# Performance work log

Hardware: AMD Instinct MI355X
Metric: run time of the kernel (lower is better)

## Reference

```python
import jax, jax.numpy as jnp
import numpy as np

IN_C = 64
OUT_C = 64
K = 3
STRIDE = 1
PAD = 1
GROUP = 1
P = 8.0
EPS = 1e-30  # guard for all-zero patch-minus-weight (never hit with randn data)


def unfold(x, k, pad, stride):
    # Torch F.unfold: output [B, C*k*k, L] with feature ordering (c, kh, kw).
    B, C, H, W = x.shape
    xp = jnp.pad(x, ((0, 0), (0, 0), (pad, pad), (pad, pad)))
    Ho = (H + 2 * pad - k) // stride + 1
    Wo = (W + 2 * pad - k) // stride + 1
    patches = jnp.stack(
        [xp[:, :, i:i + stride * Ho:stride, j:j + stride * Wo:stride]
         for i in range(k) for j in range(k)],
        axis=2,
    )  # [B, C, k*k, Ho, Wo]
    return patches.reshape(B, C * k * k, Ho * Wo), Ho, Wo


def setup_inputs() -> dict:
    key = jax.random.key(0)
    kx, kw = jax.random.split(key)
    x = jax.random.normal(kx, (2, IN_C, 32, 32), dtype=jnp.float32)
    # weight init: randn, then identity_init sets center tap to -10
    weight = jax.random.normal(kw, (OUT_C, IN_C // GROUP, K, K), dtype=jnp.float32)
    idx = jnp.arange(OUT_C)
    weight = weight.at[idx, idx % (IN_C // GROUP), K // 2, K // 2].set(-10.0)
    bias = jnp.zeros((OUT_C,), dtype=jnp.float32)
    return {"x": x, "weight": weight, "bias": bias}


def reference(x, weight, bias):
    B = x.shape[0]
    xu, Ho, Wo = unfold(x, K, PAD, STRIDE)          # [B, Cin*k*k, L]
    Kdim = (IN_C // GROUP) * K * K
    L = xu.shape[-1]
    xg = xu.reshape(B, GROUP, 1, Kdim, L)           # [B, g, 1, Kdim, L]
    wg = weight.reshape(GROUP, OUT_C // GROUP, Kdim, 1)  # [g, O/g, Kdim, 1]
    diff = jnp.abs(xg - wg)                          # [B, g, O/g, Kdim, L]
    # stable Lp norm via L-inf normalization (normalize is detached, as in torch)
    norm_inf = jax.lax.stop_gradient(jnp.max(diff, axis=3, keepdims=True))
    scaled = diff / jnp.maximum(norm_inf, EPS)
    y = jnp.sum(scaled ** P, axis=3, keepdims=True) ** (1.0 / P) * norm_inf
    y = y.reshape(B, OUT_C, Ho, Wo)
    return y + bias[None, :, None, None]
```

## Files before the change

kernel.cpp:

```cpp
#include <hip/hip_runtime.h>

#define IN_C 64
#define OUT_C 64
#define HW 32
#define PH 34

__global__ void pad_kernel(const float* __restrict__ x, float* __restrict__ xp) {
    int i = blockIdx.x * blockDim.x + threadIdx.x;
    const int total = 2 * IN_C * PH * PH;
    if (i >= total) return;
    int col = i % PH;
    int row = (i / PH) % PH;
    int bc  = i / (PH * PH);
    float v = 0.0f;
    if (row >= 1 && row <= HW && col >= 1 && col <= HW)
        v = x[bc * HW * HW + (row - 1) * HW + (col - 1)];
    xp[i] = v;
}

__global__ void wtr_kernel(const float* __restrict__ w, float* __restrict__ wt) {
    int i = blockIdx.x * blockDim.x + threadIdx.x;
    const int total = 576 * 64;
    if (i >= total) return;
    int o = i & 63;
    int ckk = i >> 6;
    wt[i] = w[o * 576 + ckk];
}

__global__ __launch_bounds__(256, 2) void norm_conv_kernel(
    const float* __restrict__ xp, const float* __restrict__ wt,
    const float* __restrict__ bias, float* __restrict__ out) {
    int bid = blockIdx.x;
    int tile = bid & 15;
    int og = (bid >> 4) & 15;
    int b = bid >> 8;

    int tid = threadIdx.x;
    int sp = tid & 63;
    int cs = __builtin_amdgcn_readfirstlane(tid >> 6);
    int row = sp >> 5, col = sp & 31;
    int oh = tile * 2 + row;
    int ow = col;

    const float* xb = xp + ((size_t)(b * IN_C + cs * 16) * PH + oh) * PH + ow;
    const float* wb = wt + (size_t)(cs * 16) * 9 * 64 + og * 4;

    float s0 = 0.f, s1 = 0.f, s2 = 0.f, s3 = 0.f;

    for (int c = 0; c < 16; ++c) {
        const float* xr = xb + c * (PH * PH);
        const float* wr = wb + c * (9 * 64);
#pragma unroll
        for (int kh = 0; kh < 3; ++kh) {
#pragma unroll
            for (int kw = 0; kw < 3; ++kw) {
                float xv = xr[kh * PH + kw];
                float4 wv = *(const float4*)(wr + (kh * 3 + kw) * 64);
                float d0 = xv - wv.x;
                float d1 = xv - wv.y;
                float d2 = xv - wv.z;
                float d3 = xv - wv.w;
                d0 *= d0; d0 *= d0; s0 = fmaf(d0, d0, s0);
                d1 *= d1; d1 *= d1; s1 = fmaf(d1, d1, s1);
                d2 *= d2; d2 *= d2; s2 = fmaf(d2, d2, s2);
                d3 *= d3; d3 *= d3; s3 = fmaf(d3, d3, s3);
            }
        }
    }

    __shared__ float lds[4 * 64 * 4];
    ((float4*)lds)[tid] = make_float4(s0, s1, s2, s3);
    __syncthreads();

    int oi = tid >> 6;
    int sp2 = tid & 63;
    float sum = lds[(0 * 64 + sp2) * 4 + oi] + lds[(1 * 64 + sp2) * 4 + oi] +
                lds[(2 * 64 + sp2) * 4 + oi] + lds[(3 * 64 + sp2) * 4 + oi];

    float y = exp2f(0.125f * log2f(sum));
    int o = og * 4 + oi;
    int oh2 = tile * 2 + (sp2 >> 5);
    int ow2 = sp2 & 31;
    out[((b * OUT_C + o) * HW + oh2) * HW + ow2] = y + bias[o];
}

extern "C" void kernel_launch(void* const* d_in, const int* in_sizes, int n_in,
                              void* d_out, int out_size, void* d_ws, size_t ws_size,
                              hipStream_t stream) {
    const float* x = (const float*)d_in[0];
    const float* w = (const float*)d_in[1];
    const float* bias = (const float*)d_in[2];
    float* out = (float*)d_out;

    float* xp = (float*)d_ws;
    float* wt = xp + 2 * IN_C * PH * PH;

    {
        int total = 2 * IN_C * PH * PH;
        pad_kernel<<<(total + 255) / 256, 256, 0, stream>>>(x, xp);
    }
    {
        int total = 576 * 64;
        wtr_kernel<<<(total + 255) / 256, 256, 0, stream>>>(w, wt);
    }
    norm_conv_kernel<<<512, 256, 0, stream>>>(xp, wt, bias, out);
}
```

Baseline: 70.12 us.

## Fuse padding and weight transpose into conv kernel with LDS staging

Removes the separate pad and weight-transpose kernels and performs both inside a single kernel. Each block stages a padded 4-row input halo for all 64 channels and its 4 output channels' weights in shared memory. Blocks grow to 512 threads with 8 channel slices, and the partial sums are reduced through padded LDS. This cuts two kernel launches and the global workspace round-trip. In exchange, every block redundantly loads its input halo, and LDS use per block is larger, which may limit occupancy.

```diff
diff --git a/kernel.cpp b/kernel.cpp
--- a/kernel.cpp
+++ b/kernel.cpp
@@ -3,59 +3,61 @@
 #define IN_C 64
 #define OUT_C 64
 #define HW 32
-#define PH 34
 
-__global__ void pad_kernel(const float* __restrict__ x, float* __restrict__ xp) {
-    int i = blockIdx.x * blockDim.x + threadIdx.x;
-    const int total = 2 * IN_C * PH * PH;
-    if (i >= total) return;
-    int col = i % PH;
-    int row = (i / PH) % PH;
-    int bc  = i / (PH * PH);
-    float v = 0.0f;
-    if (row >= 1 && row <= HW && col >= 1 && col <= HW)
-        v = x[bc * HW * HW + (row - 1) * HW + (col - 1)];
-    xp[i] = v;
-}
+#define XS_ELEMS (64 * 4 * 36)
+#define WS_ELEMS (576 * 4)
+#define RED_ELEMS (8 * 64 * 5)
 
-__global__ void wtr_kernel(const float* __restrict__ w, float* __restrict__ wt) {
-    int i = blockIdx.x * blockDim.x + threadIdx.x;
-    const int total = 576 * 64;
-    if (i >= total) return;
-    int o = i & 63;
-    int ckk = i >> 6;
-    wt[i] = w[o * 576 + ckk];
-}
+__global__ __launch_bounds__(512, 4) void norm_conv_fused(
+    const float* __restrict__ x, const float* __restrict__ w,
+    const float* __restrict__ bias, float* __restrict__ out) {
+    __shared__ float smem[XS_ELEMS + WS_ELEMS + RED_ELEMS];
+    float* xs = smem;
+    float* wsm = smem + XS_ELEMS;
+    float* red = wsm + WS_ELEMS;
 
-__global__ __launch_bounds__(256, 2) void norm_conv_kernel(
-    const float* __restrict__ xp, const float* __restrict__ wt,
-    const float* __restrict__ bias, float* __restrict__ out) {
     int bid = blockIdx.x;
     int tile = bid & 15;
     int og = (bid >> 4) & 15;
     int b = bid >> 8;
+    int tid = threadIdx.x;
 
-    int tid = threadIdx.x;
+    for (int i = tid; i < 576 * 4; i += 512) {
+        int och = i / 576;
+        int ckk = i - och * 576;
+        wsm[ckk * 4 + och] = w[(og * 4 + och) * 576 + ckk];
+    }
+
+    for (int i = tid; i < 64 * 4 * 34; i += 512) {
+        int c = i / 136;
+        int rem = i - c * 136;
+        int r = rem / 34;
+        int pc = rem - r * 34;
+        int gr = tile * 2 - 1 + r;
+        int gc = pc - 1;
+        float v = 0.0f;
+        if (gr >= 0 && gr < HW && gc >= 0 && gc < HW)
+            v = x[((b * IN_C + c) * HW + gr) * HW + gc];
+        xs[(c * 4 + r) * 36 + pc] = v;
+    }
+    __syncthreads();
+
     int sp = tid & 63;
-    int cs = __builtin_amdgcn_readfirstlane(tid >> 6);
+    int cs = tid >> 6;
     int row = sp >> 5, col = sp & 31;
-    int oh = tile * 2 + row;
-    int ow = col;
-
-    const float* xb = xp + ((size_t)(b * IN_C + cs * 16) * PH + oh) * PH + ow;
-    const float* wb = wt + (size_t)(cs * 16) * 9 * 64 + og * 4;
 
     float s0 = 0.f, s1 = 0.f, s2 = 0.f, s3 = 0.f;
 
-    for (int c = 0; c < 16; ++c) {
-        const float* xr = xb + c * (PH * PH);
-        const float* wr = wb + c * (9 * 64);
+    for (int c = 0; c < 8; ++c) {
+        int c4 = cs * 8 + c;
+        const float* xr = xs + (c4 * 4 + row) * 36 + col;
+        const float* wr = wsm + c4 * 9 * 4;
 #pragma unroll
         for (int kh = 0; kh < 3; ++kh) {
 #pragma unroll
             for (int kw = 0; kw < 3; ++kw) {
-                float xv = xr[kh * PH + kw];
-                float4 wv = *(const float4*)(wr + (kh * 3 + kw) * 64);
+                float xv = xr[kh * 36 + kw];
+                float4 wv = *(const float4*)(wr + (kh * 3 + kw) * 4);
                 float d0 = xv - wv.x;
                 float d1 = xv - wv.y;
                 float d2 = xv - wv.z;
@@ -68,20 +70,23 @@
         }
     }
 
-    __shared__ float lds[4 * 64 * 4];
-    ((float4*)lds)[tid] = make_float4(s0, s1, s2, s3);
+    float* rrow = red + (cs * 64 + sp) * 5;
+    rrow[0] = s0; rrow[1] = s1; rrow[2] = s2; rrow[3] = s3;
     __syncthreads();
 
-    int oi = tid >> 6;
-    int sp2 = tid & 63;
-    float sum = lds[(0 * 64 + sp2) * 4 + oi] + lds[(1 * 64 + sp2) * 4 + oi] +
-                lds[(2 * 64 + sp2) * 4 + oi] + lds[(3 * 64 + sp2) * 4 + oi];
-
-    float y = exp2f(0.125f * log2f(sum));
-    int o = og * 4 + oi;
-    int oh2 = tile * 2 + (sp2 >> 5);
-    int ow2 = sp2 & 31;
-    out[((b * OUT_C + o) * HW + oh2) * HW + ow2] = y + bias[o];
+    if (tid < 256) {
+        int sp2 = tid & 63;
+        int oi = tid >> 6;
+        float sum = 0.f;
+#pragma unroll
+        for (int k = 0; k < 8; ++k)
+            sum += red[(k * 64 + sp2) * 5 + oi];
+        float y = exp2f(0.125f * log2f(sum));
+        int o = og * 4 + oi;
+        int oh = tile * 2 + (sp2 >> 5);
+        int ow = sp2 & 31;
+        out[((b * OUT_C + o) * HW + oh) * HW + ow] = y + bias[o];
+    }
 }
 
 extern "C" void kernel_launch(void* const* d_in, const int* in_sizes, int n_in,
@@ -91,17 +96,5 @@
     const float* w = (const float*)d_in[1];
     const float* bias = (const float*)d_in[2];
     float* out = (float*)d_out;
-
-    float* xp = (float*)d_ws;
-    float* wt = xp + 2 * IN_C * PH * PH;
-
-    {
-        int total = 2 * IN_C * PH * PH;
-        pad_kernel<<<(total + 255) / 256, 256, 0, stream>>>(x, xp);
-    }
-    {
-        int total = 576 * 64;
-        wtr_kernel<<<(total + 255) / 256, 256, 0, stream>>>(w, wt);
-    }
-    norm_conv_kernel<<<512, 256, 0, stream>>>(xp, wt, bias, out);
+    norm_conv_fused<<<512, 512, 0, stream>>>(x, w, bias, out);
 }
```

New measurement: 70.77 us. About the same (+0.9%).
